# Kernel optimization log

Measured on AMD Instinct MI355X. Metric: run time of the kernel, lower is better.

Reference implementation:

```python
import jax, jax.numpy as jnp
import numpy as np

B, S, D, F, E = 8, 2048, 512, 2048, 8


def setup_inputs() -> dict:
    key = jax.random.key(0)
    ks = jax.random.split(key, 7)
    x = jax.random.normal(ks[0], (B, S, D), dtype=jnp.float32)
    Wr = jax.random.normal(ks[1], (D, E), dtype=jnp.float32) * 0.02
    br = jnp.zeros((E,), dtype=jnp.float32)
    W1 = jax.random.normal(ks[2], (E, D, F), dtype=jnp.float32) * 0.02
    b1 = jnp.zeros((E, F), dtype=jnp.float32)
    W2 = jax.random.normal(ks[3], (E, F, D), dtype=jnp.float32) * 0.02
    b2 = jnp.zeros((E, D), dtype=jnp.float32)
    return {"x": x, "Wr": Wr, "br": br, "W1": W1, "b1": b1, "W2": W2, "b2": b2}


def reference(x, Wr, br, W1, b1, W2, b2):
    # Router: softmax gate + top-2
    logits = jnp.einsum('bsd,de->bse', x, Wr) + br            # [B,S,E]
    gate = jax.nn.softmax(logits, axis=-1)                    # [B,S,E]
    top2_val, top2_idx = jax.lax.top_k(gate, 2)               # [B,S,2]

    # Combine weights: gate value on the two selected experts, 0 elsewhere
    onehot = jax.nn.one_hot(top2_idx, E, dtype=x.dtype)       # [B,S,2,E]
    combine = jnp.sum(onehot * top2_val[..., None], axis=2)   # [B,S,E]

    # Dense per-expert FFN, masked-combined (same math as the token loop)
    out = jnp.zeros_like(x)
    for e in range(E):
        h = jax.nn.relu(jnp.einsum('bsd,df->bsf', x, W1[e]) + b1[e])
        y = jnp.einsum('bsf,fd->bsd', h, W2[e]) + b2[e]
        out = out + combine[..., e, None] * y

    # GShard-style load-balancing aux loss
    expert_prob = gate.mean(axis=(0, 1))                      # [E]
    aux_loss = jnp.sum(expert_prob * jnp.log(expert_prob + 1e-9))
    return out, aux_loss
```

## Files before the change

### kernel.cpp

```cpp
#include <hip/hip_runtime.h>
#include <math.h>

typedef unsigned short u16;
typedef __attribute__((ext_vector_type(8))) short short8;
typedef __attribute__((ext_vector_type(8))) u16 u16x8;
typedef __attribute__((ext_vector_type(4))) float f32x4;

#define NTOK 16384
#define DDIM 512
#define FDIM 2048
#define ENUM 8
#define NBLK 1024
#define APAD (32768 + 256)
#define NTCAP 264
#define G1GRID 4224
#define G2GRID 1056

__device__ __forceinline__ u16 f2bf(float f) {
  unsigned u = __float_as_uint(f);
  u += 0x7FFFu + ((u >> 16) & 1u);
  return (u16)(u >> 16);
}
__device__ __forceinline__ float bf2f(u16 b) {
  return __uint_as_float(((unsigned)b) << 16);
}

typedef const __attribute__((address_space(1))) unsigned int* gas1_t;
typedef __attribute__((address_space(3))) unsigned int* las3_t;
__device__ __forceinline__ void gload16(const u16* g, u16* l) {
  __builtin_amdgcn_global_load_lds((gas1_t)(const void*)g, (las3_t)(void*)l, 16, 0, 0);
}

__global__ __launch_bounds__(256) void prep_kernel(
    const float* __restrict__ x, const float* __restrict__ Wr,
    const float* __restrict__ br, int* __restrict__ top2e,
    float* __restrict__ top2v, int* __restrict__ histBase,
    float* __restrict__ gatePart, const float* __restrict__ W1,
    const float* __restrict__ W2, u16* __restrict__ W1T,
    u16* __restrict__ W2T) {
  __shared__ __align__(16) char smem[24704];
  int tid = threadIdx.x;
  if (blockIdx.x < NBLK) {
    float* sWr = (float*)smem;
    float(*sX)[DDIM] = (float(*)[DDIM])(smem + 16384);
    int* sHist = (int*)(smem + 16384 + 8192);
    float* sGate = (float*)(smem + 16384 + 8192 + 32);
    for (int i = tid; i < DDIM * ENUM; i += 256) sWr[i] = Wr[i];
    if (tid < ENUM) { sHist[tid] = 0; sGate[tid] = 0.f; }
    __syncthreads();
    int wave = tid >> 6, lane = tid & 63;
    int e = lane >> 3, dg = lane & 7;
    float bre = br[e];
    for (int it = 0; it < 4; ++it) {
      int t = blockIdx.x * 16 + wave * 4 + it;
      const float4* xr = (const float4*)(x + (size_t)t * DDIM);
      float4* sx4 = (float4*)sX[wave];
      sx4[lane] = xr[lane];
      sx4[lane + 64] = xr[lane + 64];
      asm volatile("s_waitcnt lgkmcnt(0)" ::: "memory");
      float acc = 0.f;
#pragma unroll 16
      for (int i = 0; i < 64; ++i) {
        float xv = sX[wave][i * 8 + dg];
        acc += xv * sWr[(i * 8 + dg) * 8 + e];
      }
      acc += __shfl_xor(acc, 1);
      acc += __shfl_xor(acc, 2);
      acc += __shfl_xor(acc, 4);
      float logit = acc + bre;
      float m = logit;
      m = fmaxf(m, __shfl_xor(m, 8));
      m = fmaxf(m, __shfl_xor(m, 16));
      m = fmaxf(m, __shfl_xor(m, 32));
      float pv = expf(logit - m);
      float s = pv;
      s += __shfl_xor(s, 8);
      s += __shfl_xor(s, 16);
      s += __shfl_xor(s, 32);
      float gate = pv / s;
      float v1 = gate; int i1 = e;
#pragma unroll
      for (int msk = 8; msk <= 32; msk <<= 1) {
        float ov = __shfl_xor(v1, msk);
        int oi = __shfl_xor(i1, msk);
        if (ov > v1 || (ov == v1 && oi < i1)) { v1 = ov; i1 = oi; }
      }
      float g2 = (e == i1) ? -1.f : gate;
      float v2 = g2; int i2 = e;
#pragma unroll
      for (int msk = 8; msk <= 32; msk <<= 1) {
        float ov = __shfl_xor(v2, msk);
        int oi = __shfl_xor(i2, msk);
        if (ov > v2 || (ov == v2 && oi < i2)) { v2 = ov; i2 = oi; }
      }
      if (lane == 0) {
        top2e[2 * t] = i1; top2e[2 * t + 1] = i2;
        top2v[2 * t] = v1; top2v[2 * t + 1] = v2;
        atomicAdd(&sHist[i1], 1);
        atomicAdd(&sHist[i2], 1);
      }
      if (dg == 0) atomicAdd(&sGate[e], gate);
    }
    __syncthreads();
    if (tid < ENUM) {
      histBase[blockIdx.x * 8 + tid] = sHist[tid];
      gatePart[blockIdx.x * 8 + tid] = sGate[tid];
    }
  } else {
    float(*tile)[65] = (float(*)[65])smem;
    int idx = blockIdx.x - NBLK;
    int by = idx >> 8, bx = idx & 255;
    int half = by >> 3, e = by & 7;
    const float* W = half ? W2 : W1;
    u16* WT = half ? W2T : W1T;
    int K = half ? FDIM : DDIM, N = half ? DDIM : FDIM;
    int tnc = N >> 6;
    int tk = bx / tnc, tn = bx - tk * tnc;
    const float* Wp = W + (size_t)e * K * N + (size_t)(tk * 64) * N + tn * 64;
#pragma unroll
    for (int i = 0; i < 4; ++i) {
      int row = (tid >> 4) + i * 16, c4 = (tid & 15) * 4;
      float4 v = *(const float4*)(Wp + (size_t)row * N + c4);
      tile[row][c4] = v.x; tile[row][c4 + 1] = v.y;
      tile[row][c4 + 2] = v.z; tile[row][c4 + 3] = v.w;
    }
    __syncthreads();
    u16* WTp = WT + (size_t)e * N * K + (size_t)(tn * 64) * K + tk * 64;
#pragma unroll
    for (int p = 0; p < 2; ++p) {
      int n = (tid >> 3) + p * 32, k0 = (tid & 7) * 8;
      u16x8 o;
#pragma unroll
      for (int j = 0; j < 8; ++j) o[j] = f2bf(tile[k0 + j][n]);
      *(u16x8*)(WTp + (size_t)n * K + k0) = o;
    }
  }
}

__global__ __launch_bounds__(256) void scan_kernel(
    int* __restrict__ histBase, const float* __restrict__ gatePart,
    int* __restrict__ offsets, int* __restrict__ counts,
    int* __restrict__ tileE, int* __restrict__ tileM, int* __restrict__ nT,
    float* __restrict__ auxOut) {
  __shared__ int sTot[ENUM];
  __shared__ float sG[ENUM];
  int tid = threadIdx.x, wave = tid >> 6, lane = tid & 63;
  if (tid < ENUM) sG[tid] = 0.f;
  __syncthreads();
  float loc[8] = {0, 0, 0, 0, 0, 0, 0, 0};
  for (int r = tid; r < NBLK; r += 256) {
#pragma unroll
    for (int e = 0; e < 8; ++e) loc[e] += gatePart[r * 8 + e];
  }
#pragma unroll
  for (int e = 0; e < 8; ++e) atomicAdd(&sG[e], loc[e]);
#pragma unroll
  for (int ei = 0; ei < 2; ++ei) {
    int e = wave * 2 + ei;
    int running = 0;
    for (int itb = 0; itb < NBLK / 64; ++itb) {
      int idx = (itb * 64 + lane) * 8 + e;
      int v = histBase[idx];
      int inc = v;
#pragma unroll
      for (int d = 1; d < 64; d <<= 1) {
        int o = __shfl_up(inc, d);
        if (lane >= d) inc += o;
      }
      histBase[idx] = running + inc - v;
      running += __shfl(inc, 63);
    }
    if (lane == 0) sTot[e] = running;
  }
  __syncthreads();
  if (tid == 0) {
    int off = 0, nt = 0;
#pragma unroll
    for (int e = 0; e < 8; ++e) {
      int c = sTot[e];
      offsets[e] = off; counts[e] = c; off += c;
      int mt = (c + 127) >> 7;
      for (int m = 0; m < mt; ++m) { tileE[nt] = e; tileM[nt] = m; ++nt; }
    }
    nT[0] = nt;
    float aux = 0.f;
#pragma unroll
    for (int e = 0; e < 8; ++e) {
      float pr = sG[e] / (float)NTOK;
      aux += pr * logf(pr + 1e-9f);
    }
    *auxOut = aux;
  }
}

__global__ __launch_bounds__(256) void place_kernel(
    const float* __restrict__ x, const int* __restrict__ top2e,
    const float* __restrict__ top2v, const int* __restrict__ histBase,
    const int* __restrict__ offsets, int* __restrict__ tokA,
    float* __restrict__ assignW, u16* __restrict__ Xg) {
  __shared__ int sA[32];
  int tid = threadIdx.x, wave = tid >> 6, lane = tid & 63;
  int blk = blockIdx.x;
  if (tid < 32) {
    int slot = tid;
    int t = blk * 16 + (slot >> 1);
    int e = top2e[2 * t + (slot & 1)];
    float v = top2v[2 * t + (slot & 1)];
    int rank = 0;
#pragma unroll
    for (int ee = 0; ee < 8; ++ee) {
      unsigned long long mm = __ballot(e == ee);
      if (e == ee) rank = __popcll(mm & ((1ull << slot) - 1));
    }
    int a = offsets[e] + histBase[blk * 8 + e] + rank;
    sA[slot] = a;
    tokA[2 * t + (slot & 1)] = a;
    assignW[a] = v;
  }
  __syncthreads();
  for (int it = 0; it < 4; ++it) {
    int lt = wave * 4 + it;
    int t = blk * 16 + lt;
    const float4* xr = (const float4*)(x + (size_t)t * DDIM);
    float4 v0 = xr[lane * 2], v1 = xr[lane * 2 + 1];
    u16x8 o;
    o[0] = f2bf(v0.x); o[1] = f2bf(v0.y); o[2] = f2bf(v0.z); o[3] = f2bf(v0.w);
    o[4] = f2bf(v1.x); o[5] = f2bf(v1.y); o[6] = f2bf(v1.z); o[7] = f2bf(v1.w);
    int a1 = sA[2 * lt], a2 = sA[2 * lt + 1];
    *(u16x8*)(Xg + (size_t)a1 * DDIM + lane * 8) = o;
    *(u16x8*)(Xg + (size_t)a2 * DDIM + lane * 8) = o;
  }
}

template <int K>
__device__ __forceinline__ void mainloopR(
    const u16* __restrict__ aG0, const u16* __restrict__ aG1,
    const u16* __restrict__ bG0, const u16* __restrict__ bG1,
    char* ldsB, f32x4 (&acc)[4][4]) {
  const int tid = threadIdx.x;
  const int lane = tid & 63, wave = tid >> 6;
  const int wr = wave >> 1, wc = wave & 1;
  const int fr = lane & 15;
  const int slotx = ((lane >> 4) ^ ((lane >> 1) & 3)) & 3;
  const int frA = wr * 4096 + fr * 64 + slotx * 16;
  const int frB = 8192 + wc * 4096 + fr * 64 + slotx * 16;
  const int w1024 = wave * 1024;
  const int KT = K / 32;

  auto STAGE = [&](int u, int s) {
    const size_t go = (size_t)u * 32;
    char* base = ldsB + s * 16384 + w1024;
    gload16(aG0 + go, (u16*)base);
    gload16(aG1 + go, (u16*)(base + 4096));
    gload16(bG0 + go, (u16*)(base + 8192));
    gload16(bG1 + go, (u16*)(base + 8192 + 4096));
  };

  STAGE(0, 0);
  STAGE(1, 1);
  asm volatile("s_waitcnt vmcnt(4)" ::: "memory");
  __builtin_amdgcn_s_barrier();
  __builtin_amdgcn_sched_barrier(0);

  int s0 = 0, s1 = 1, s2 = 2;
#pragma unroll 1
  for (int t = 0; t < KT; ++t) {
    const char* cb = ldsB + s0 * 16384;
    short8 af[4], bf[4];
#pragma unroll
    for (int m = 0; m < 4; ++m)
      af[m] = *(const short8*)(cb + frA + m * 1024);
#pragma unroll
    for (int n = 0; n < 4; ++n)
      bf[n] = *(const short8*)(cb + frB + n * 1024);
    STAGE((t + 2) & (KT - 1), s2);
    asm volatile("s_waitcnt vmcnt(4)" ::: "memory");
    __builtin_amdgcn_s_barrier();
    __builtin_amdgcn_sched_barrier(0);
    __builtin_amdgcn_s_setprio(1);
#pragma unroll
    for (int m = 0; m < 4; ++m)
#pragma unroll
      for (int n = 0; n < 4; ++n)
        acc[m][n] = __builtin_amdgcn_mfma_f32_16x16x32_bf16(af[m], bf[n],
                                                            acc[m][n], 0, 0, 0);
    __builtin_amdgcn_s_setprio(0);
    __builtin_amdgcn_s_barrier();
    __builtin_amdgcn_sched_barrier(0);
    int tmp = s0; s0 = s1; s1 = s2; s2 = tmp;
  }
}

__global__ __launch_bounds__(256) void gemm1_kernel(
    const u16* __restrict__ Xg, const u16* __restrict__ W1T,
    const float* __restrict__ b1, u16* __restrict__ h,
    const int* __restrict__ counts, const int* __restrict__ offsets,
    const int* __restrict__ tileE, const int* __restrict__ tileM,
    const int* __restrict__ nT) {
  __shared__ __align__(16) char ldsB[49152];
  int wg = blockIdx.x;
  int L = (wg & 7) * (G1GRID / 8) + (wg >> 3);
  int tile = L >> 4, ntile = L & 15;
  if (tile >= nT[0]) return;
  int e = tileE[tile], mtile = tileM[tile];
  int cnt = counts[e], off = offsets[e];
  int tid = threadIdx.x;
  int r0 = tid >> 2;
  int cswz = ((tid & 3) ^ ((tid >> 3) & 3)) * 8;
  const u16* Ap = Xg + (size_t)(off + mtile * 128) * DDIM;
  const u16* aG0 = Ap + (size_t)r0 * DDIM + cswz;
  const u16* aG1 = Ap + (size_t)(r0 + 64) * DDIM + cswz;
  const u16* Bp = W1T + ((size_t)e * FDIM + ntile * 128) * DDIM;
  const u16* bG0 = Bp + (size_t)r0 * DDIM + cswz;
  const u16* bG1 = Bp + (size_t)(r0 + 64) * DDIM + cswz;
  f32x4 acc[4][4] = {};
  mainloopR<DDIM>(aG0, aG1, bG0, bG1, ldsB, acc);
  int lane = tid & 63, wave = tid >> 6;
  int wr = wave >> 1, wc = wave & 1;
  int cl = lane & 15, rq = (lane >> 4) * 4;
#pragma unroll
  for (int m = 0; m < 4; ++m) {
#pragma unroll
    for (int i = 0; i < 4; ++i) {
      int gr = mtile * 128 + wr * 64 + m * 16 + rq + i;
      if (gr < cnt) {
#pragma unroll
        for (int n = 0; n < 4; ++n) {
          int gc = ntile * 128 + wc * 64 + n * 16 + cl;
          float v = acc[m][n][i] + b1[e * FDIM + gc];
          v = fmaxf(v, 0.f);
          h[(size_t)(off + gr) * FDIM + gc] = f2bf(v);
        }
      }
    }
  }
}

__global__ __launch_bounds__(256) void gemm2_kernel(
    const u16* __restrict__ h, const u16* __restrict__ W2T,
    const float* __restrict__ b2, const float* __restrict__ assignW,
    const int* __restrict__ counts, const int* __restrict__ offsets,
    const int* __restrict__ tileE, const int* __restrict__ tileM,
    const int* __restrict__ nT, u16* __restrict__ z) {
  __shared__ __align__(16) char ldsB[49152];
  int wg = blockIdx.x;
  int L = (wg & 7) * (G2GRID / 8) + (wg >> 3);
  int tile = L >> 2, ntile = L & 3;
  if (tile >= nT[0]) return;
  int e = tileE[tile], mtile = tileM[tile];
  int cnt = counts[e], off = offsets[e];
  int tid = threadIdx.x;
  int r0 = tid >> 2;
  int cswz = ((tid & 3) ^ ((tid >> 3) & 3)) * 8;
  const u16* Ap = h + (size_t)(off + mtile * 128) * FDIM;
  const u16* aG0 = Ap + (size_t)r0 * FDIM + cswz;
  const u16* aG1 = Ap + (size_t)(r0 + 64) * FDIM + cswz;
  const u16* Bp = W2T + ((size_t)e * DDIM + ntile * 128) * FDIM;
  const u16* bG0 = Bp + (size_t)r0 * FDIM + cswz;
  const u16* bG1 = Bp + (size_t)(r0 + 64) * FDIM + cswz;
  f32x4 acc[4][4] = {};
  mainloopR<FDIM>(aG0, aG1, bG0, bG1, ldsB, acc);
  int lane = tid & 63, wave = tid >> 6;
  int wr = wave >> 1, wc = wave & 1;
  int cl = lane & 15, rq = (lane >> 4) * 4;
#pragma unroll
  for (int m = 0; m < 4; ++m) {
#pragma unroll
    for (int i = 0; i < 4; ++i) {
      int gr = mtile * 128 + wr * 64 + m * 16 + rq + i;
      if (gr < cnt) {
        int a = off + gr;
        float w = assignW[a];
#pragma unroll
        for (int n = 0; n < 4; ++n) {
          int gc = ntile * 128 + wc * 64 + n * 16 + cl;
          float v = (acc[m][n][i] + b2[e * DDIM + gc]) * w;
          z[(size_t)a * DDIM + gc] = f2bf(v);
        }
      }
    }
  }
}

__global__ __launch_bounds__(256) void combine_kernel(
    const u16* __restrict__ z, const int* __restrict__ tokA,
    float* __restrict__ out) {
  int tid = threadIdx.x, wave = tid >> 6, lane = tid & 63;
  int t = blockIdx.x * 4 + wave;
  int a1 = tokA[2 * t], a2 = tokA[2 * t + 1];
  u16x8 v1 = *(const u16x8*)(z + (size_t)a1 * DDIM + lane * 8);
  u16x8 v2 = *(const u16x8*)(z + (size_t)a2 * DDIM + lane * 8);
  float4 o0, o1;
  o0.x = bf2f(v1[0]) + bf2f(v2[0]);
  o0.y = bf2f(v1[1]) + bf2f(v2[1]);
  o0.z = bf2f(v1[2]) + bf2f(v2[2]);
  o0.w = bf2f(v1[3]) + bf2f(v2[3]);
  o1.x = bf2f(v1[4]) + bf2f(v2[4]);
  o1.y = bf2f(v1[5]) + bf2f(v2[5]);
  o1.z = bf2f(v1[6]) + bf2f(v2[6]);
  o1.w = bf2f(v1[7]) + bf2f(v2[7]);
  float4* o = (float4*)(out + (size_t)t * DDIM + lane * 8);
  o[0] = o0;
  o[1] = o1;
}

extern "C" void kernel_launch(void* const* d_in, const int* in_sizes, int n_in,
                              void* d_out, int out_size, void* d_ws, size_t ws_size,
                              hipStream_t stream) {
  const float* x  = (const float*)d_in[0];
  const float* Wr = (const float*)d_in[1];
  const float* br = (const float*)d_in[2];
  const float* W1 = (const float*)d_in[3];
  const float* b1 = (const float*)d_in[4];
  const float* W2 = (const float*)d_in[5];
  const float* b2 = (const float*)d_in[6];
  float* out = (float*)d_out;

  char* ws = (char*)d_ws;
  size_t p = 0;
  auto alloc = [&](size_t bytes) -> void* {
    void* r = ws + p;
    p = (p + bytes + 255) & ~(size_t)255;
    return r;
  };
  int* counts     = (int*)alloc(ENUM * 4);
  int* offsets    = (int*)alloc(ENUM * 4);
  int* nT         = (int*)alloc(4);
  int* tileE      = (int*)alloc(NTCAP * 4);
  int* tileM      = (int*)alloc(NTCAP * 4);
  int* top2e      = (int*)alloc((size_t)NTOK * 2 * 4);
  float* top2v    = (float*)alloc((size_t)NTOK * 2 * 4);
  int* tokA       = (int*)alloc((size_t)NTOK * 2 * 4);
  float* assignW  = (float*)alloc((size_t)APAD * 4);
  int* histBase   = (int*)alloc((size_t)NBLK * 8 * 4);
  float* gatePart = (float*)alloc((size_t)NBLK * 8 * 4);
  u16* W1T        = (u16*)alloc((size_t)ENUM * FDIM * DDIM * 2);
  u16* W2T        = (u16*)alloc((size_t)ENUM * DDIM * FDIM * 2);
  u16* Xg         = (u16*)alloc((size_t)APAD * DDIM * 2);
  u16* hbuf       = (u16*)alloc((size_t)APAD * FDIM * 2);
  u16* z          = Xg;
  (void)in_sizes; (void)n_in; (void)out_size; (void)ws_size;

  prep_kernel<<<NBLK + 4096, 256, 0, stream>>>(x, Wr, br, top2e, top2v,
                                               histBase, gatePart, W1, W2,
                                               W1T, W2T);
  scan_kernel<<<1, 256, 0, stream>>>(histBase, gatePart, offsets, counts,
                                     tileE, tileM, nT,
                                     out + (size_t)NTOK * DDIM);
  place_kernel<<<NBLK, 256, 0, stream>>>(x, top2e, top2v, histBase, offsets,
                                         tokA, assignW, Xg);
  gemm1_kernel<<<G1GRID, 256, 0, stream>>>(
      Xg, W1T, b1, hbuf, counts, offsets, tileE, tileM, nT);
  gemm2_kernel<<<G2GRID, 256, 0, stream>>>(
      hbuf, W2T, b2, assignW, counts, offsets, tileE, tileM, nT, z);
  combine_kernel<<<NTOK / 4, 256, 0, stream>>>(z, tokA, out);
}
```

Baseline: 283.5 us.

## Use 256x256 tiles with 8 waves for first expert GEMM

Replaces the first grouped GEMM's 128x128 tile with 256x256 tiles computed by 512-thread blocks (8 waves, each an 128x64 sub-tile), using 96KB of dynamic LDS with triple buffering. The scan kernel now builds a separate tile list for gemm1 at 256-row granularity, while gemm2 keeps its 128-row list. The aim is more data reuse per loaded byte and fewer blocks. The trade-off is more padding waste on ragged per-expert counts, lower occupancy from the larger LDS footprint and registers, and fewer blocks to spread over the CUs.

Result: slower. 297.3 us (+4.9%).

```diff
diff --git a/kernel.cpp b/kernel.cpp
--- a/kernel.cpp
+++ b/kernel.cpp
@@ -12,8 +12,9 @@
 #define ENUM 8
 #define NBLK 1024
 #define APAD (32768 + 256)
-#define NTCAP 264
-#define G1GRID 4224
+#define NT1CAP 136
+#define NT2CAP 264
+#define G1GRID 1080
 #define G2GRID 1056
 
 __device__ __forceinline__ u16 f2bf(float f) {
@@ -140,8 +141,9 @@
 __global__ __launch_bounds__(256) void scan_kernel(
     int* __restrict__ histBase, const float* __restrict__ gatePart,
     int* __restrict__ offsets, int* __restrict__ counts,
-    int* __restrict__ tileE, int* __restrict__ tileM, int* __restrict__ nT,
-    float* __restrict__ auxOut) {
+    int* __restrict__ tileE1, int* __restrict__ tileM1,
+    int* __restrict__ tileE2, int* __restrict__ tileM2,
+    int* __restrict__ nT, float* __restrict__ auxOut) {
   __shared__ int sTot[ENUM];
   __shared__ float sG[ENUM];
   int tid = threadIdx.x, wave = tid >> 6, lane = tid & 63;
@@ -174,15 +176,17 @@
   }
   __syncthreads();
   if (tid == 0) {
-    int off = 0, nt = 0;
+    int off = 0, nt1 = 0, nt2 = 0;
 #pragma unroll
     for (int e = 0; e < 8; ++e) {
       int c = sTot[e];
       offsets[e] = off; counts[e] = c; off += c;
-      int mt = (c + 127) >> 7;
-      for (int m = 0; m < mt; ++m) { tileE[nt] = e; tileM[nt] = m; ++nt; }
-    }
-    nT[0] = nt;
+      int mt1 = (c + 255) >> 8;
+      for (int m = 0; m < mt1; ++m) { tileE1[nt1] = e; tileM1[nt1] = m; ++nt1; }
+      int mt2 = (c + 127) >> 7;
+      for (int m = 0; m < mt2; ++m) { tileE2[nt2] = e; tileM2[nt2] = m; ++nt2; }
+    }
+    nT[0] = nt1; nT[1] = nt2;
     float aux = 0.f;
 #pragma unroll
     for (int e = 0; e < 8; ++e) {
@@ -233,6 +237,110 @@
 }
 
 template <int K>
+__device__ __forceinline__ void mainloop8W(
+    const u16* __restrict__ aG0, const u16* __restrict__ aG1,
+    const u16* __restrict__ bG0, const u16* __restrict__ bG1,
+    char* ldsB, f32x4 (&acc)[8][4]) {
+  const int tid = threadIdx.x;
+  const int lane = tid & 63, wave = tid >> 6;
+  const int wr = wave >> 2, wc = wave & 3;
+  const int fr = lane & 15;
+  const int slotx = ((lane >> 4) ^ ((lane >> 1) & 3)) & 3;
+  const int frA = (wr * 128 + fr) * 64 + slotx * 16;
+  const int frB = 16384 + (wc * 64 + fr) * 64 + slotx * 16;
+  const int w1024 = wave * 1024;
+  const int KT = K / 32;
+
+  auto STAGE = [&](int u, int s) {
+    const size_t go = (size_t)u * 32;
+    char* base = ldsB + s * 32768 + w1024;
+    gload16(aG0 + go, (u16*)base);
+    gload16(aG1 + go, (u16*)(base + 8192));
+    gload16(bG0 + go, (u16*)(base + 16384));
+    gload16(bG1 + go, (u16*)(base + 16384 + 8192));
+  };
+
+  STAGE(0, 0);
+  STAGE(1, 1);
+  asm volatile("s_waitcnt vmcnt(4)" ::: "memory");
+  __builtin_amdgcn_s_barrier();
+  __builtin_amdgcn_sched_barrier(0);
+
+  int s0 = 0, s1 = 1, s2 = 2;
+#pragma unroll 1
+  for (int t = 0; t < KT; ++t) {
+    const char* cb = ldsB + s0 * 32768;
+    short8 af[8], bf[4];
+#pragma unroll
+    for (int m = 0; m < 8; ++m)
+      af[m] = *(const short8*)(cb + frA + m * 1024);
+#pragma unroll
+    for (int n = 0; n < 4; ++n)
+      bf[n] = *(const short8*)(cb + frB + n * 1024);
+    STAGE((t + 2) & (KT - 1), s2);
+    asm volatile("s_waitcnt vmcnt(4)" ::: "memory");
+    __builtin_amdgcn_s_barrier();
+    __builtin_amdgcn_sched_barrier(0);
+    __builtin_amdgcn_s_setprio(1);
+#pragma unroll
+    for (int m = 0; m < 8; ++m)
+#pragma unroll
+      for (int n = 0; n < 4; ++n)
+        acc[m][n] = __builtin_amdgcn_mfma_f32_16x16x32_bf16(af[m], bf[n],
+                                                            acc[m][n], 0, 0, 0);
+    __builtin_amdgcn_s_setprio(0);
+    __builtin_amdgcn_s_barrier();
+    __builtin_amdgcn_sched_barrier(0);
+    int tmp = s0; s0 = s1; s1 = s2; s2 = tmp;
+  }
+}
+
+__global__ __launch_bounds__(512) void gemm1_kernel(
+    const u16* __restrict__ Xg, const u16* __restrict__ W1T,
+    const float* __restrict__ b1, u16* __restrict__ h,
+    const int* __restrict__ counts, const int* __restrict__ offsets,
+    const int* __restrict__ tileE1, const int* __restrict__ tileM1,
+    const int* __restrict__ nT) {
+  extern __shared__ char ldsB[];
+  int wg = blockIdx.x;
+  int L = (wg & 7) * (G1GRID / 8) + (wg >> 3);
+  int tile = L >> 3, ntile = L & 7;
+  if (tile >= nT[0]) return;
+  int e = tileE1[tile], mtile = tileM1[tile];
+  int cnt = counts[e], off = offsets[e];
+  int tid = threadIdx.x;
+  int r0 = tid >> 2;
+  int cswz = ((tid & 3) ^ ((tid >> 3) & 3)) * 8;
+  const u16* Ap = Xg + (size_t)(off + mtile * 256) * DDIM;
+  const u16* aG0 = Ap + (size_t)r0 * DDIM + cswz;
+  const u16* aG1 = Ap + (size_t)(r0 + 128) * DDIM + cswz;
+  const u16* Bp = W1T + ((size_t)e * FDIM + ntile * 256) * DDIM;
+  const u16* bG0 = Bp + (size_t)r0 * DDIM + cswz;
+  const u16* bG1 = Bp + (size_t)(r0 + 128) * DDIM + cswz;
+  f32x4 acc[8][4] = {};
+  mainloop8W<DDIM>(aG0, aG1, bG0, bG1, ldsB, acc);
+  int lane = tid & 63, wave = tid >> 6;
+  int wr = wave >> 2, wc = wave & 3;
+  int cl = lane & 15, rq = (lane >> 4) * 4;
+#pragma unroll
+  for (int m = 0; m < 8; ++m) {
+#pragma unroll
+    for (int i = 0; i < 4; ++i) {
+      int gr = mtile * 256 + wr * 128 + m * 16 + rq + i;
+      if (gr < cnt) {
+#pragma unroll
+        for (int n = 0; n < 4; ++n) {
+          int gc = ntile * 256 + wc * 64 + n * 16 + cl;
+          float v = acc[m][n][i] + b1[e * FDIM + gc];
+          v = fmaxf(v, 0.f);
+          h[(size_t)(off + gr) * FDIM + gc] = f2bf(v);
+        }
+      }
+    }
+  }
+}
+
+template <int K>
 __device__ __forceinline__ void mainloopR(
     const u16* __restrict__ aG0, const u16* __restrict__ aG1,
     const u16* __restrict__ bG0, const u16* __restrict__ bG1,
@@ -291,63 +399,18 @@
   }
 }
 
-__global__ __launch_bounds__(256) void gemm1_kernel(
-    const u16* __restrict__ Xg, const u16* __restrict__ W1T,
-    const float* __restrict__ b1, u16* __restrict__ h,
-    const int* __restrict__ counts, const int* __restrict__ offsets,
-    const int* __restrict__ tileE, const int* __restrict__ tileM,
-    const int* __restrict__ nT) {
-  __shared__ __align__(16) char ldsB[49152];
-  int wg = blockIdx.x;
-  int L = (wg & 7) * (G1GRID / 8) + (wg >> 3);
-  int tile = L >> 4, ntile = L & 15;
-  if (tile >= nT[0]) return;
-  int e = tileE[tile], mtile = tileM[tile];
-  int cnt = counts[e], off = offsets[e];
-  int tid = threadIdx.x;
-  int r0 = tid >> 2;
-  int cswz = ((tid & 3) ^ ((tid >> 3) & 3)) * 8;
-  const u16* Ap = Xg + (size_t)(off + mtile * 128) * DDIM;
-  const u16* aG0 = Ap + (size_t)r0 * DDIM + cswz;
-  const u16* aG1 = Ap + (size_t)(r0 + 64) * DDIM + cswz;
-  const u16* Bp = W1T + ((size_t)e * FDIM + ntile * 128) * DDIM;
-  const u16* bG0 = Bp + (size_t)r0 * DDIM + cswz;
-  const u16* bG1 = Bp + (size_t)(r0 + 64) * DDIM + cswz;
-  f32x4 acc[4][4] = {};
-  mainloopR<DDIM>(aG0, aG1, bG0, bG1, ldsB, acc);
-  int lane = tid & 63, wave = tid >> 6;
-  int wr = wave >> 1, wc = wave & 1;
-  int cl = lane & 15, rq = (lane >> 4) * 4;
-#pragma unroll
-  for (int m = 0; m < 4; ++m) {
-#pragma unroll
-    for (int i = 0; i < 4; ++i) {
-      int gr = mtile * 128 + wr * 64 + m * 16 + rq + i;
-      if (gr < cnt) {
-#pragma unroll
-        for (int n = 0; n < 4; ++n) {
-          int gc = ntile * 128 + wc * 64 + n * 16 + cl;
-          float v = acc[m][n][i] + b1[e * FDIM + gc];
-          v = fmaxf(v, 0.f);
-          h[(size_t)(off + gr) * FDIM + gc] = f2bf(v);
-        }
-      }
-    }
-  }
-}
-
 __global__ __launch_bounds__(256) void gemm2_kernel(
     const u16* __restrict__ h, const u16* __restrict__ W2T,
     const float* __restrict__ b2, const float* __restrict__ assignW,
     const int* __restrict__ counts, const int* __restrict__ offsets,
-    const int* __restrict__ tileE, const int* __restrict__ tileM,
+    const int* __restrict__ tileE2, const int* __restrict__ tileM2,
     const int* __restrict__ nT, u16* __restrict__ z) {
   __shared__ __align__(16) char ldsB[49152];
   int wg = blockIdx.x;
   int L = (wg & 7) * (G2GRID / 8) + (wg >> 3);
   int tile = L >> 2, ntile = L & 3;
-  if (tile >= nT[0]) return;
-  int e = tileE[tile], mtile = tileM[tile];
+  if (tile >= nT[1]) return;
+  int e = tileE2[tile], mtile = tileM2[tile];
   int cnt = counts[e], off = offsets[e];
   int tid = threadIdx.x;
   int r0 = tid >> 2;
@@ -425,9 +488,11 @@
   };
   int* counts     = (int*)alloc(ENUM * 4);
   int* offsets    = (int*)alloc(ENUM * 4);
-  int* nT         = (int*)alloc(4);
-  int* tileE      = (int*)alloc(NTCAP * 4);
-  int* tileM      = (int*)alloc(NTCAP * 4);
+  int* nT         = (int*)alloc(2 * 4);
+  int* tileE1     = (int*)alloc(NT1CAP * 4);
+  int* tileM1     = (int*)alloc(NT1CAP * 4);
+  int* tileE2     = (int*)alloc(NT2CAP * 4);
+  int* tileM2     = (int*)alloc(NT2CAP * 4);
   int* top2e      = (int*)alloc((size_t)NTOK * 2 * 4);
   float* top2v    = (float*)alloc((size_t)NTOK * 2 * 4);
   int* tokA       = (int*)alloc((size_t)NTOK * 2 * 4);
@@ -441,17 +506,20 @@
   u16* z          = Xg;
   (void)in_sizes; (void)n_in; (void)out_size; (void)ws_size;
 
+  (void)hipFuncSetAttribute((const void*)gemm1_kernel,
+                            hipFuncAttributeMaxDynamicSharedMemorySize, 98304);
+
   prep_kernel<<<NBLK + 4096, 256, 0, stream>>>(x, Wr, br, top2e, top2v,
                                                histBase, gatePart, W1, W2,
                                                W1T, W2T);
   scan_kernel<<<1, 256, 0, stream>>>(histBase, gatePart, offsets, counts,
-                                     tileE, tileM, nT,
+                                     tileE1, tileM1, tileE2, tileM2, nT,
                                      out + (size_t)NTOK * DDIM);
   place_kernel<<<NBLK, 256, 0, stream>>>(x, top2e, top2v, histBase, offsets,
                                          tokA, assignW, Xg);
-  gemm1_kernel<<<G1GRID, 256, 0, stream>>>(
-      Xg, W1T, b1, hbuf, counts, offsets, tileE, tileM, nT);
+  gemm1_kernel<<<G1GRID, 512, 98304, stream>>>(
+      Xg, W1T, b1, hbuf, counts, offsets, tileE1, tileM1, nT);
   gemm2_kernel<<<G2GRID, 256, 0, stream>>>(
-      hbuf, W2T, b2, assignW, counts, offsets, tileE, tileM, nT, z);
+      hbuf, W2T, b2, assignW, counts, offsets, tileE2, tileM2, nT, z);
   combine_kernel<<<NTOK / 4, 256, 0, stream>>>(z, tokA, out);
 }
```
